# Optimization experiments

Hardware: AMD Instinct MI355X
Metric: run time of the kernel (lower is better)

Reference implementation:

```python
import jax, jax.numpy as jnp
import numpy as np

# Dimensions inferred from VSSBlockOneWay(hidden_dim=256, ssm_d_state=64, forward_type='m0_noz')
B_, L_, D_ = 8, 2048, 256      # batch, seq_len, d_model
DIN, N_, P_ = 512, 64, 64      # d_inner = 2*d_model, d_state, head_dim
H_ = DIN // P_                 # n_heads = 8


def _ln(x, w, b, eps=1e-5):
    m = x.mean(-1, keepdims=True)
    v = ((x - m) ** 2).mean(-1, keepdims=True)
    return (x - m) * jax.lax.rsqrt(v + eps) * w + b


def setup_inputs() -> dict:
    key = jax.random.key(0)
    ks = jax.random.split(key, 8)
    s = lambda k, shape, sc: jax.random.normal(k, shape, jnp.float32) * sc
    return dict(
        src=jax.random.normal(ks[0], (B_, L_, D_), jnp.float32),
        ln_w=jnp.ones((D_,), jnp.float32), ln_b=jnp.zeros((D_,), jnp.float32),
        W_in=s(ks[1], (D_, DIN), 0.02),
        conv_w=s(ks[2], (DIN, 1, 3), 0.1),            # depthwise conv1d kernel
        conv_b=jnp.zeros((DIN,), jnp.float32),
        W_xproj=s(ks[3], (DIN, H_ + 2 * N_), 0.02),   # -> (dt | B | C)
        dt_bias=s(ks[4], (H_,), 0.1),
        A_log=jnp.log(jnp.arange(1, H_ + 1, dtype=jnp.float32)),  # Mamba2 A-init
        Ds=jnp.ones((H_,), jnp.float32),
        oln_w=jnp.ones((DIN,), jnp.float32), oln_b=jnp.zeros((DIN,), jnp.float32),
        W_out=s(ks[5], (DIN, D_), 0.02),
    )


def reference(src, ln_w, ln_b, W_in, conv_w, conv_b, W_xproj, dt_bias,
              A_log, Ds, oln_w, oln_b, W_out):
    B, L, D = src.shape
    H, N, P = H_, N_, P_
    x = _ln(src, ln_w, ln_b)
    u = x @ W_in                                                    # (B,L,DIN)
    # depthwise conv over sequence, SAME padding (VMamba uses non-causal dwconv)
    uc = jax.lax.conv_general_dilated(
        u.transpose(0, 2, 1), conv_w, (1,), 'SAME',
        feature_group_count=DIN, dimension_numbers=('NCH', 'OIH', 'NCH'))
    u = jax.nn.gelu((uc + conv_b[None, :, None]).transpose(0, 2, 1),
                    approximate=False)                              # (B,L,DIN)
    dbc = u @ W_xproj                                               # (B,L,H+2N)
    dt = jax.nn.softplus(dbc[..., :H] + dt_bias)                    # (B,L,H)
    Bm = dbc[..., H:H + N]                                          # (B,L,N)
    Cm = dbc[..., H + N:]                                           # (B,L,N)
    A = -jnp.exp(A_log)                                             # (H,)
    decay = jnp.exp(dt * A)                                         # (B,L,H)
    xh = u.reshape(B, L, H, P)
    dtx = dt[..., None] * xh                                        # (B,L,H,P)

    def step(h, inp):
        dec_t, dtx_t, B_t, C_t = inp
        # h: (B,H,P,N)
        h = h * dec_t[:, :, None, None] + dtx_t[..., None] * B_t[:, None, None, :]
        y = jnp.einsum('bhpn,bn->bhp', h, C_t)
        return h, y

    h0 = jnp.zeros((B, H, P, N), u.dtype)
    inputs = (decay.transpose(1, 0, 2), dtx.transpose(1, 0, 2, 3),
              Bm.transpose(1, 0, 2), Cm.transpose(1, 0, 2))
    _, ys = jax.lax.scan(step, h0, inputs)                          # (L,B,H,P)
    y = ys.transpose(1, 0, 2, 3) + xh * Ds[None, None, :, None]
    y = _ln(y.reshape(B, L, DIN), oln_w, oln_b)
    # dropout / drop_path are identity at inference
    return src + y @ W_out
```

## Files before the change

kernel.cpp:

```cpp
#include <hip/hip_runtime.h>
#include <hip/hip_bf16.h>
#include <cmath>

typedef __hip_bfloat16 bf16;
typedef short bf16x8 __attribute__((ext_vector_type(8)));
typedef short bf16x4v __attribute__((ext_vector_type(4)));
typedef float f32x4 __attribute__((ext_vector_type(4)));

constexpr int B_ = 8, L_ = 2048, D_ = 256, DIN_ = 512;
constexpr int H_ = 8, N_ = 64, P_ = 64;
constexpr int BL_ = B_ * L_;
constexpr int NCH_ = 136;
constexpr int Q_ = 64;
constexpr int NC_ = L_ / Q_;

static __device__ __forceinline__ float b2f(bf16 x) { return __bfloat162float(x); }
static __device__ __forceinline__ bf16  f2b(float x) { return __float2bfloat16(x); }
static __device__ __forceinline__ bf16  rawb(short s) { __hip_bfloat16_raw r; r.x = (unsigned short)s; return (bf16)r; }
static __device__ __forceinline__ float sane(float v) { return (fabsf(v) <= 1e30f) ? v : 0.f; }
static __device__ __forceinline__ float loadx(const void* p, size_t i, bool isbf) {
    return isbf ? b2f(((const bf16*)p)[i]) : ((const float*)p)[i];
}
static __device__ __forceinline__ bf16x8 load8x(const void* p, size_t off, bool isbf) {
    if (isbf) return *(const bf16x8*)((const bf16*)p + off);
    const float4* fp = (const float4*)((const float*)p + off);
    float4 f0 = fp[0], f1 = fp[1];
    bf16 t[8] = {f2b(f0.x), f2b(f0.y), f2b(f0.z), f2b(f0.w),
                 f2b(f1.x), f2b(f1.y), f2b(f1.z), f2b(f1.w)};
    return *(bf16x8*)t;
}
static __device__ __forceinline__ int swz(int row, int col) { return col ^ (((row >> 3) & 7) * 8); }

static __device__ __forceinline__ f32x4 mfma16(bf16x8 a, bf16x8 b, f32x4 c) {
    return __builtin_amdgcn_mfma_f32_16x16x32_bf16(a, b, c, 0, 0, 0);
}
#define ONES8 bf16x8{16256, 16256, 16256, 16256, 16256, 16256, 16256, 16256}

__global__ __launch_bounds__(256) void prep_k(const void* __restrict__ Win, const void* __restrict__ Wx,
                       const void* __restrict__ Wo,
                       const void* __restrict__ ln_w, const void* __restrict__ ln_b,
                       const void* __restrict__ oln_w, const void* __restrict__ oln_b,
                       bf16* __restrict__ WinT, bf16* __restrict__ WxT, bf16* __restrict__ WoT,
                       float* __restrict__ colsum1, float* __restrict__ bias1,
                       float* __restrict__ colsum2, float* __restrict__ bias2,
                       const unsigned short* __restrict__ flagp) {
    const bool isbf = flagp[0] != 0;
    const int bx = blockIdx.x, tid = threadIdx.x;
    if (bx < 88) {
        __shared__ float T[64][65];
        if (bx < 32) {
            int d0 = (bx & 3) * 64, n0 = (bx >> 2) * 64;
#pragma unroll
            for (int i = 0; i < 16; i++) {
                int e = tid + 256 * i; int r = e >> 6, c = e & 63;
                T[r][c] = loadx(Win, (size_t)(d0 + r) * DIN_ + n0 + c, isbf);
            }
            __syncthreads();
#pragma unroll
            for (int i = 0; i < 16; i++) {
                int e = tid + 256 * i; int r = e >> 6, c = e & 63;
                WinT[(size_t)(n0 + r) * D_ + d0 + c] = f2b(loadx(ln_w, d0 + c, isbf) * T[c][r]);
            }
        } else if (bx < 64) {
            int t2 = bx - 32;
            int k0 = (t2 & 7) * 64, d0 = (t2 >> 3) * 64;
#pragma unroll
            for (int i = 0; i < 16; i++) {
                int e = tid + 256 * i; int r = e >> 6, c = e & 63;
                T[r][c] = loadx(Wo, (size_t)(k0 + r) * D_ + d0 + c, isbf);
            }
            __syncthreads();
#pragma unroll
            for (int i = 0; i < 16; i++) {
                int e = tid + 256 * i; int r = e >> 6, c = e & 63;
                WoT[(size_t)(d0 + r) * DIN_ + k0 + c] = f2b(loadx(oln_w, k0 + c, isbf) * T[c][r]);
            }
        } else {
            int t3 = bx - 64;
            int i0 = (t3 & 7) * 64, j0 = (t3 >> 3) * 64;
#pragma unroll
            for (int i = 0; i < 16; i++) {
                int e = tid + 256 * i; int r = e >> 6, c = e & 63;
                int j = j0 + c;
                T[r][c] = (j < NCH_) ? loadx(Wx, (size_t)(i0 + r) * NCH_ + j, isbf) : 0.f;
            }
            __syncthreads();
#pragma unroll
            for (int i = 0; i < 16; i++) {
                int e = tid + 256 * i; int r = e >> 6, c = e & 63;
                WxT[(size_t)(j0 + r) * DIN_ + i0 + c] = f2b(T[c][r]);
            }
        }
        return;
    }
    const int o = (bx - 88) * 4 + (tid >> 6);
    const int lane = tid & 63;
    float cs = 0.f, bs = 0.f;
    if (o < DIN_) {
        int n = o;
        for (int i = lane; i < D_; i += 64) {
            float wv = loadx(Win, (size_t)i * DIN_ + n, isbf);
            cs += loadx(ln_w, i, isbf) * wv;
            bs += loadx(ln_b, i, isbf) * wv;
        }
    } else {
        int d = o - DIN_;
        for (int k = lane; k < DIN_; k += 64) {
            float wv = loadx(Wo, (size_t)k * D_ + d, isbf);
            cs += loadx(oln_w, k, isbf) * wv;
            bs += loadx(oln_b, k, isbf) * wv;
        }
    }
#pragma unroll
    for (int off = 32; off >= 1; off >>= 1) { cs += __shfl_xor(cs, off); bs += __shfl_xor(bs, off); }
    if (lane == 0) {
        if (o < DIN_) { colsum1[o] = cs; bias1[o] = bs; }
        else          { colsum2[o - DIN_] = cs; bias2[o - DIN_] = bs; }
    }
}

__global__ __launch_bounds__(256) void gemm1_k(const void* __restrict__ src,
                                               const bf16* __restrict__ WinT,
                                               const float* __restrict__ colsum1,
                                               const float* __restrict__ bias1,
                                               bf16* __restrict__ u0,
                                               const unsigned short* __restrict__ flagp) {
    const bool isbf = flagp[0] != 0;
    constexpr int K = D_;
    constexpr int STR = K + 8;
    constexpr int CH = K / 8;
    __shared__ bf16 Blds[64 * STR];
    const int tid = threadIdx.x;
    const int n0 = blockIdx.y * 64;
#pragma unroll
    for (int i = 0; i < 64 * CH / 256; i++) {
        int e = tid + 256 * i;
        int r = e / CH, cch = e % CH;
        bf16x8 v = *(const bf16x8*)(WinT + (size_t)(n0 + r) * K + cch * 8);
        *(bf16x8*)(&Blds[r * STR + cch * 8]) = v;
    }
    __syncthreads();
    const int wave = tid >> 6, lane = tid & 63;
    const int quad = lane >> 4, l16 = lane & 15;
    const int m0 = blockIdx.x * 128 + wave * 32;
    const bf16x8 ones = ONES8;
    f32x4 acc[2][4], accS[2], accS2[2];
#pragma unroll
    for (int i = 0; i < 2; i++) {
        accS[i] = f32x4{0.f, 0.f, 0.f, 0.f};
        accS2[i] = f32x4{0.f, 0.f, 0.f, 0.f};
#pragma unroll
        for (int j = 0; j < 4; j++) acc[i][j] = f32x4{0.f, 0.f, 0.f, 0.f};
    }
    const size_t r0 = (size_t)(m0 + l16) * K + quad * 8;
    const size_t r1 = r0 + (size_t)16 * K;
#pragma unroll
    for (int k0 = 0; k0 < K; k0 += 32) {
        bf16x8 a0 = load8x(src, r0 + k0, isbf);
        bf16x8 a1 = load8x(src, r1 + k0, isbf);
        accS[0]  = mfma16(a0, ones, accS[0]);
        accS2[0] = mfma16(a0, a0, accS2[0]);
        accS[1]  = mfma16(a1, ones, accS[1]);
        accS2[1] = mfma16(a1, a1, accS2[1]);
#pragma unroll
        for (int i = 0; i < 4; i++) {
            bf16x8 bb = *(const bf16x8*)(&Blds[(16 * i + l16) * STR + k0 + quad * 8]);
            acc[0][i] = mfma16(a0, bb, acc[0][i]);
            acc[1][i] = mfma16(a1, bb, acc[1][i]);
        }
    }
    float cs[4], bsv[4];
#pragma unroll
    for (int i = 0; i < 4; i++) { int n = n0 + 16 * i + l16; cs[i] = colsum1[n]; bsv[i] = bias1[n]; }
#pragma unroll
    for (int rb = 0; rb < 2; rb++)
#pragma unroll
        for (int r = 0; r < 4; r++) {
            int rl = quad * 4 + r;
            float sv  = accS[rb][r];
            float s2v = __shfl(accS2[rb][r], (quad << 4) + rl);
            float mean = sv * (1.f / D_);
            float var  = s2v * (1.f / D_) - mean * mean;
            float rs = rsqrtf(fmaxf(var, 0.f) + 1e-5f);
            int m = m0 + rb * 16 + rl;
#pragma unroll
            for (int i = 0; i < 4; i++) {
                int n = n0 + 16 * i + l16;
                float v = rs * (acc[rb][i][r] - mean * cs[i]) + bsv[i];
                u0[(size_t)m * DIN_ + n] = f2b(v);
            }
        }
}

template<int MODE>
__global__ __launch_bounds__(256) void gemmB_k(const bf16* __restrict__ A,
                                               const bf16* __restrict__ BT,
                                               void* __restrict__ Cout,
                                               const void* __restrict__ resid,
                                               const float* __restrict__ colsum,
                                               const float* __restrict__ biasv,
                                               const void* __restrict__ dt_bias,
                                               const void* __restrict__ A_log,
                                               float* __restrict__ dtg,
                                               float* __restrict__ dtAg,
                                               const unsigned short* __restrict__ flagp) {
    const bool isbf = flagp[0] != 0;
    constexpr int K = 512;
    constexpr int KH = 256;
    constexpr int STR = KH + 8;
    constexpr int CH = KH / 8;
    __shared__ bf16 Blds[64 * STR];
    const int tid = threadIdx.x;
    const int n0 = blockIdx.y * 64;
    const int wave = tid >> 6, lane = tid & 63;
    const int quad = lane >> 4, l16 = lane & 15;
    const int m0 = blockIdx.x * 128 + wave * 32;
    const bf16x8 ones = ONES8;
    f32x4 acc[2][4], accS[2], accS2[2];
#pragma unroll
    for (int i = 0; i < 2; i++) {
        accS[i] = f32x4{0.f, 0.f, 0.f, 0.f};
        accS2[i] = f32x4{0.f, 0.f, 0.f, 0.f};
#pragma unroll
        for (int j = 0; j < 4; j++) acc[i][j] = f32x4{0.f, 0.f, 0.f, 0.f};
    }
    const bf16* a0p = A + (size_t)(m0 + l16) * K + quad * 8;
    const bf16* a1p = a0p + (size_t)16 * K;
#pragma unroll
    for (int kh = 0; kh < 2; kh++) {
        if (kh) __syncthreads();
#pragma unroll
        for (int i = 0; i < 64 * CH / 256; i++) {
            int e = tid + 256 * i;
            int r = e / CH, cch = e % CH;
            bf16x8 v = *(const bf16x8*)(BT + (size_t)(n0 + r) * K + kh * KH + cch * 8);
            *(bf16x8*)(&Blds[r * STR + cch * 8]) = v;
        }
        __syncthreads();
        const bf16* ah0 = a0p + kh * KH;
        const bf16* ah1 = a1p + kh * KH;
#pragma unroll 4
        for (int k0 = 0; k0 < KH; k0 += 32) {
            bf16x8 a0 = *(const bf16x8*)(ah0 + k0);
            bf16x8 a1 = *(const bf16x8*)(ah1 + k0);
            if (MODE == 1) {
                accS[0]  = mfma16(a0, ones, accS[0]);
                accS2[0] = mfma16(a0, a0, accS2[0]);
                accS[1]  = mfma16(a1, ones, accS[1]);
                accS2[1] = mfma16(a1, a1, accS2[1]);
            }
#pragma unroll
            for (int i = 0; i < 4; i++) {
                bf16x8 bb = *(const bf16x8*)(&Blds[(16 * i + l16) * STR + k0 + quad * 8]);
                acc[0][i] = mfma16(a0, bb, acc[0][i]);
                acc[1][i] = mfma16(a1, bb, acc[1][i]);
            }
        }
    }
    if (MODE == 0) {
#pragma unroll
        for (int rb = 0; rb < 2; rb++)
#pragma unroll
            for (int r = 0; r < 4; r++) {
                int m = m0 + rb * 16 + quad * 4 + r;
#pragma unroll
                for (int i = 0; i < 4; i++) {
                    int n = n0 + 16 * i + l16;
                    if (n < NCH_) ((bf16*)Cout)[(size_t)m * NCH_ + n] = f2b(acc[rb][i][r]);
                }
            }
        if (blockIdx.y == 0 && l16 < 8) {
            float bb = loadx(dt_bias, l16, isbf);
            float Ah = -__expf(fminf(loadx(A_log, l16, isbf), 30.f));
#pragma unroll
            for (int rb = 0; rb < 2; rb++)
#pragma unroll
                for (int r = 0; r < 4; r++) {
                    int m = m0 + rb * 16 + quad * 4 + r;
                    float raw = acc[rb][0][r] + bb;
                    float sp = raw > 20.f ? raw : log1pf(__expf(raw));
                    sp = fminf(sp, 60.f);
                    dtg[(size_t)m * H_ + l16]  = sp;
                    dtAg[(size_t)m * H_ + l16] = sp * Ah;
                }
        }
    } else {
        float cs[4], bsv[4];
#pragma unroll
        for (int i = 0; i < 4; i++) { int n = n0 + 16 * i + l16; cs[i] = colsum[n]; bsv[i] = biasv[n]; }
#pragma unroll
        for (int rb = 0; rb < 2; rb++)
#pragma unroll
            for (int r = 0; r < 4; r++) {
                int rl = quad * 4 + r;
                float sv  = accS[rb][r];
                float s2v = __shfl(accS2[rb][r], (quad << 4) + rl);
                float mean = sv * (1.f / K);
                float var  = s2v * (1.f / K) - mean * mean;
                float rs = rsqrtf(fmaxf(var, 0.f) + 1e-5f);
                int m = m0 + rb * 16 + rl;
#pragma unroll
                for (int i = 0; i < 4; i++) {
                    int n = n0 + 16 * i + l16;
                    size_t o = (size_t)m * D_ + n;
                    float v = rs * (acc[rb][i][r] - mean * cs[i]) + bsv[i] + loadx(resid, o, isbf);
                    v = sane(v);
                    if (isbf) ((bf16*)Cout)[o] = f2b(v);
                    else      ((float*)Cout)[o] = v;
                }
            }
    }
}

constexpr int CSTRIP_ = 4;
__global__ __launch_bounds__(256) void conv_k(const bf16* __restrict__ u0,
                                              const void* __restrict__ cw,
                                              const void* __restrict__ cb,
                                              bf16* __restrict__ u,
                                              const unsigned short* __restrict__ flagp) {
    const bool isbf = flagp[0] != 0;
    __shared__ float wlds[2048];
    {
        int t = threadIdx.x;
#pragma unroll
        for (int i = 0; i < 6; i++) { int e = t + 256 * i; wlds[e] = loadx(cw, e, isbf); }
        wlds[t + 1536] = loadx(cb, t, isbf);
        wlds[t + 1792] = loadx(cb, t + 256, isbf);
    }
    __syncthreads();
    const int wave = threadIdx.x >> 6, lane = threadIdx.x & 63;
    const int sid = blockIdx.x * 4 + wave;
    const int bl0 = sid * CSTRIP_;
    const int l0 = bl0 & (L_ - 1);
    const int c8 = lane * 8;
    float w0[8], w1[8], w2[8], bias[8];
#pragma unroll
    for (int t = 0; t < 8; t++) {
        int ch = c8 + t;
        w0[t] = wlds[ch * 3 + 0];
        w1[t] = wlds[ch * 3 + 1];
        w2[t] = wlds[ch * 3 + 2];
        bias[t] = wlds[1536 + ch];
    }
    const bf16x8* rp = (const bf16x8*)(u0 + (size_t)bl0 * DIN_ + c8);
    bf16x8 zero = {0, 0, 0, 0, 0, 0, 0, 0};
    bf16x8 vl = (l0 > 0) ? rp[-64] : zero;
    bf16x8 vm = rp[0];
#pragma unroll
    for (int i = 0; i < CSTRIP_; i++) {
        int l = l0 + i;
        bf16x8 vr = (l < L_ - 1) ? rp[64 * (i + 1)] : zero;
        bf16 ob[8];
#pragma unroll
        for (int t = 0; t < 8; t++) {
            float a = bias[t] + w1[t] * b2f(rawb(vm[t]))
                    + w0[t] * b2f(rawb(vl[t])) + w2[t] * b2f(rawb(vr[t]));
            float ge = 0.5f * a * (1.f + erff(a * 0.70710678118f));
            ob[t] = f2b(ge);
        }
        *(bf16x8*)(u + (size_t)(bl0 + i) * DIN_ + c8) = *(bf16x8*)ob;
        vl = vm; vm = vr;
    }
}

__global__ __launch_bounds__(256) void chunk_state_k(const bf16* __restrict__ ubuf,
                                                     const bf16* __restrict__ dbcb,
                                                     const float* __restrict__ dtg,
                                                     const float* __restrict__ dtAg,
                                                     bf16* __restrict__ HS,
                                                     float* __restrict__ cdg) {
    const int idx = blockIdx.x;
    const int c = idx & 31, h = (idx >> 5) & 7, b = idx >> 8;
    const int bh = b * 8 + h;
    const int blbase = b * L_ + c * Q_;
    __shared__ bf16 Xw[64][72];
    __shared__ bf16 BTb[64][72];
    __shared__ float fj[64];
    const int tid = threadIdx.x;
    if (tid < 64) {
        int j = tid;
        float dA  = dtAg[(size_t)(blbase + j) * H_ + h];
        float dtv = dtg[(size_t)(blbase + j) * H_ + h];
        float v = dA;
#pragma unroll
        for (int off = 1; off < 64; off <<= 1) { float t = __shfl_up(v, off); if (j >= off) v += t; }
        float segEnd = __shfl(v, 63);
        fj[j] = __expf(fminf(segEnd - v, 0.f)) * dtv;
        if (j == 0) cdg[bh * NC_ + c] = __expf(fminf(segEnd, 0.f));
    }
    __syncthreads();
    {
        const int jr = tid >> 3, p8 = (tid & 7) * 8;
#pragma unroll
        for (int it = 0; it < 2; it++) {
            int j = jr + 32 * it;
            float fs = fj[j];
            bf16x8 xv = *(const bf16x8*)(ubuf + (size_t)(blbase + j) * DIN_ + h * 64 + p8);
            bf16x8 bv = *(const bf16x8*)(dbcb + (size_t)(blbase + j) * NCH_ + 8 + p8);
#pragma unroll
            for (int t = 0; t < 8; t++) {
                int p = p8 + t;
                Xw[p][swz(p, j)]  = f2b(fs * b2f(rawb(xv[t])));
                BTb[p][swz(p, j)] = rawb(bv[t]);
            }
        }
    }
    __syncthreads();
    const int wave = tid >> 6, lane = tid & 63, quad = lane >> 4, l16 = lane & 15;
    const int p0 = wave * 16;
    f32x4 acc[4];
#pragma unroll
    for (int i = 0; i < 4; i++) acc[i] = f32x4{0.f, 0.f, 0.f, 0.f};
#pragma unroll
    for (int ks = 0; ks < 2; ks++) {
        int pa = p0 + l16;
        bf16x8 a = *(const bf16x8*)(&Xw[pa][swz(pa, ks * 32 + quad * 8)]);
#pragma unroll
        for (int nt = 0; nt < 4; nt++) {
            int nb = nt * 16 + l16;
            bf16x8 bb = *(const bf16x8*)(&BTb[nb][swz(nb, ks * 32 + quad * 8)]);
            acc[nt] = mfma16(a, bb, acc[nt]);
        }
    }
    size_t slot = (size_t)(bh * NC_ + c) * 4096;
#pragma unroll
    for (int nt = 0; nt < 4; nt++)
#pragma unroll
        for (int r = 0; r < 4; r++) {
            int p = p0 + quad * 4 + r, n = nt * 16 + l16;
            HS[slot + p * 64 + n] = f2b(sane(acc[nt][r]));
        }
}

__global__ __launch_bounds__(256) void chunk_rec_k(bf16* __restrict__ HS,
                                                   const float* __restrict__ cdg) {
    const int bh = blockIdx.x >> 2, sub = blockIdx.x & 3;
    const int eo = sub * 1024 + threadIdx.x * 4;
    bf16* base = HS + (size_t)bh * (NC_ * 4096) + eo;
    bf16x4v v[NC_];
#pragma unroll
    for (int c = 0; c < NC_; c++) v[c] = *(const bf16x4v*)(base + (size_t)c * 4096);
    float cdr[NC_];
#pragma unroll
    for (int c = 0; c < NC_; c++) cdr[c] = cdg[bh * NC_ + c];
    float h0 = 0.f, h1 = 0.f, h2 = 0.f, h3 = 0.f;
#pragma unroll
    for (int c = 0; c < NC_; c++) {
        bf16 ob[4] = {f2b(h0), f2b(h1), f2b(h2), f2b(h3)};
        *(bf16x4v*)(base + (size_t)c * 4096) = *(bf16x4v*)ob;
        float cd = cdr[c];
        h0 = cd * h0 + b2f(rawb(v[c][0]));
        h1 = cd * h1 + b2f(rawb(v[c][1]));
        h2 = cd * h2 + b2f(rawb(v[c][2]));
        h3 = cd * h3 + b2f(rawb(v[c][3]));
    }
}

__global__ __launch_bounds__(256) void chunk_out_k(bf16* __restrict__ ubuf,
                                                   const bf16* __restrict__ dbcb,
                                                   const float* __restrict__ dtg,
                                                   const float* __restrict__ dtAg,
                                                   const bf16* __restrict__ HS,
                                                   const void* __restrict__ Ds,
                                                   bf16* __restrict__ ybuf,
                                                   const unsigned short* __restrict__ flagp) {
    const bool isbf = flagp[0] != 0;
    const int idx = blockIdx.x;
    const int c = idx & 31, h = (idx >> 5) & 7, b = idx >> 8;
    const int bh = b * 8 + h;
    const int blbase = b * L_ + c * Q_;
    const size_t slotbase = (size_t)(bh * NC_ + c) * 4096;
    __shared__ bf16 Xb[64][72];
    __shared__ bf16 Gb[64][72];
    __shared__ float segL[64], PL[64], dtL[64];
    const int tid = threadIdx.x;
    if (tid < 64) {
        int j = tid;
        float dA  = dtAg[(size_t)(blbase + j) * H_ + h];
        float dtv = dtg[(size_t)(blbase + j) * H_ + h];
        float v = dA;
#pragma unroll
        for (int off = 1; off < 64; off <<= 1) { float t = __shfl_up(v, off); if (j >= off) v += t; }
        segL[j] = v;
        PL[j]   = __expf(fminf(v, 0.f));
        dtL[j]  = dtv;
    }
    {
        const int rr = tid >> 3, k8 = (tid & 7) * 8;
#pragma unroll
        for (int it = 0; it < 2; it++) {
            int r = rr + 32 * it;
            bf16x8 xv = *(const bf16x8*)(ubuf + (size_t)(blbase + r) * DIN_ + h * 64 + k8);
#pragma unroll
            for (int t = 0; t < 8; t++) { int p = k8 + t; Xb[p][swz(p, r)] = rawb(xv[t]); }
        }
    }
    __syncthreads();
    const int wave = tid >> 6, lane = tid & 63, quad = lane >> 4, l16 = lane & 15;
    const int l0 = wave * 16;
    f32x4 g[4];
#pragma unroll
    for (int i = 0; i < 4; i++) g[i] = f32x4{0.f, 0.f, 0.f, 0.f};
#pragma unroll
    for (int ks = 0; ks < 2; ks++) {
        bf16x8 a = *(const bf16x8*)(dbcb + (size_t)(blbase + l0 + l16) * NCH_ + 72 + ks * 32 + quad * 8);
#pragma unroll
        for (int jt = 0; jt < 4; jt++) {
            bf16x8 bb = *(const bf16x8*)(dbcb + (size_t)(blbase + jt * 16 + l16) * NCH_ + 8 + ks * 32 + quad * 8);
            g[jt] = mfma16(a, bb, g[jt]);
        }
    }
#pragma unroll
    for (int jt = 0; jt < 4; jt++) {
        int j = jt * 16 + l16;
#pragma unroll
        for (int r = 0; r < 4; r++) {
            int l = l0 + quad * 4 + r;
            float e = __expf(fminf(segL[l] - segL[j], 0.f));
            float gv = (j <= l) ? sane(g[jt][r]) * e * dtL[j] : 0.f;
            Gb[l][swz(l, j)] = f2b(sane(gv));
        }
    }
    __syncthreads();
    f32x4 y1[4], y2[4];
#pragma unroll
    for (int i = 0; i < 4; i++) { y1[i] = f32x4{0.f, 0.f, 0.f, 0.f}; y2[i] = f32x4{0.f, 0.f, 0.f, 0.f}; }
#pragma unroll
    for (int ks = 0; ks < 2; ks++) {
        int la = l0 + l16;
        bf16x8 ag = *(const bf16x8*)(&Gb[la][swz(la, ks * 32 + quad * 8)]);
        bf16x8 ac = *(const bf16x8*)(dbcb + (size_t)(blbase + la) * NCH_ + 72 + ks * 32 + quad * 8);
#pragma unroll
        for (int pt = 0; pt < 4; pt++) {
            int pb = pt * 16 + l16;
            bf16x8 bx = *(const bf16x8*)(&Xb[pb][swz(pb, ks * 32 + quad * 8)]);
            bf16x8 bhf = *(const bf16x8*)(HS + slotbase + (size_t)pb * 64 + ks * 32 + quad * 8);
            y1[pt] = mfma16(ag, bx, y1[pt]);
            y2[pt] = mfma16(ac, bhf, y2[pt]);
        }
    }
    float dsH = loadx(Ds, h, isbf);
#pragma unroll
    for (int pt = 0; pt < 4; pt++) {
        int p = pt * 16 + l16;
#pragma unroll
        for (int r = 0; r < 4; r++) {
            int l = l0 + quad * 4 + r;
            float yv = y1[pt][r] + PL[l] * y2[pt][r] + dsH * b2f(Xb[p][swz(p, l)]);
            ybuf[(size_t)(blbase + l) * DIN_ + h * 64 + p] = f2b(sane(yv));
        }
    }
}

extern "C" void kernel_launch(void* const* d_in, const int* in_sizes, int n_in,
                              void* d_out, int out_size, void* d_ws, size_t ws_size,
                              hipStream_t stream) {
    const void* src     = d_in[0];
    const void* ln_w    = d_in[1];
    const void* ln_b    = d_in[2];
    const void* W_in    = d_in[3];
    const void* conv_w  = d_in[4];
    const void* conv_b  = d_in[5];
    const void* W_xproj = d_in[6];
    const void* dt_bias = d_in[7];
    const void* A_log   = d_in[8];
    const void* Ds      = d_in[9];
    const void* oln_w   = d_in[10];
    const void* oln_b   = d_in[11];
    const void* W_out   = d_in[12];
    const unsigned short* flagp = (const unsigned short*)ln_w;

    char* w = (char*)d_ws;
    size_t off = 0;
    auto alloc = [&](size_t bytes) { void* p = w + off; off += (bytes + 255) & ~(size_t)255; return p; };
    char*   regB   = (char*)alloc((size_t)BL_ * DIN_ * 2);
    char*   regC   = (char*)alloc((size_t)BL_ * DIN_ * 2);
    bf16*   dbcb   = (bf16*)alloc((size_t)BL_ * NCH_ * 2);
    float*  dtg    = (float*)alloc((size_t)BL_ * H_ * 4);
    float*  dtAg   = (float*)alloc((size_t)BL_ * H_ * 4);
    bf16*   WinT   = (bf16*)alloc((size_t)DIN_ * D_ * 2);
    bf16*   WxT    = (bf16*)alloc((size_t)192 * DIN_ * 2);
    bf16*   WoT    = (bf16*)alloc((size_t)D_ * DIN_ * 2);
    float*  colsum1= (float*)alloc(DIN_ * 4);
    float*  bias1  = (float*)alloc(DIN_ * 4);
    float*  colsum2= (float*)alloc(D_ * 4);
    float*  bias2  = (float*)alloc(D_ * 4);
    float*  cdg    = (float*)alloc((size_t)64 * NC_ * 4);

    bf16* u0buf = (bf16*)regB;
    bf16* HS    = (bf16*)regB;
    bf16* ubuf  = (bf16*)regC;
    bf16* ybuf  = (bf16*)regC;

    prep_k<<<88 + 192, 256, 0, stream>>>(W_in, W_xproj, W_out, ln_w, ln_b, oln_w, oln_b,
                                         WinT, WxT, WoT, colsum1, bias1, colsum2, bias2, flagp);
    gemm1_k<<<dim3(BL_ / 128, 8), 256, 0, stream>>>(src, WinT, colsum1, bias1, u0buf, flagp);
    conv_k<<<BL_ / CSTRIP_ / 4, 256, 0, stream>>>(u0buf, conv_w, conv_b, ubuf, flagp);
    gemmB_k<0><<<dim3(BL_ / 128, 3), 256, 0, stream>>>(ubuf, WxT, dbcb, nullptr, nullptr, nullptr,
                                                       dt_bias, A_log, dtg, dtAg, flagp);
    chunk_state_k<<<B_ * H_ * NC_, 256, 0, stream>>>(ubuf, dbcb, dtg, dtAg, HS, cdg);
    chunk_rec_k<<<256, 256, 0, stream>>>(HS, cdg);
    chunk_out_k<<<B_ * H_ * NC_, 256, 0, stream>>>(ubuf, dbcb, dtg, dtAg, HS, Ds, ybuf, flagp);
    gemmB_k<1><<<dim3(BL_ / 128, 4), 256, 0, stream>>>(ybuf, WoT, d_out, src, colsum2, bias2,
                                                       nullptr, nullptr, nullptr, nullptr, flagp);
}
```

Baseline: 199.0 us.

## Fuse input GEMM with depthwise conv and GELU via LDS halo rows

Merges the LayerNorm+input-projection GEMM with the depthwise conv and GELU into one kernel. The GEMM tile is staged in shared memory, and the two halo rows at the tile edges are recomputed with a scalar dot product over the staged weight slice. This removes the intermediate u0 write and read plus one kernel launch. In exchange it adds extra shared memory per block, serial halo work for 128 threads, and another barrier.

```diff
diff --git a/kernel.cpp b/kernel.cpp
--- a/kernel.cpp
+++ b/kernel.cpp
@@ -119,19 +119,24 @@
     }
 }
 
-__global__ __launch_bounds__(256) void gemm1_k(const void* __restrict__ src,
-                                               const bf16* __restrict__ WinT,
-                                               const float* __restrict__ colsum1,
-                                               const float* __restrict__ bias1,
-                                               bf16* __restrict__ u0,
-                                               const unsigned short* __restrict__ flagp) {
+__global__ __launch_bounds__(256) void gemm1conv_k(const void* __restrict__ src,
+                                                   const bf16* __restrict__ WinT,
+                                                   const float* __restrict__ colsum1,
+                                                   const float* __restrict__ bias1,
+                                                   const void* __restrict__ cw,
+                                                   const void* __restrict__ cb,
+                                                   bf16* __restrict__ u,
+                                                   const unsigned short* __restrict__ flagp) {
     const bool isbf = flagp[0] != 0;
     constexpr int K = D_;
     constexpr int STR = K + 8;
     constexpr int CH = K / 8;
     __shared__ bf16 Blds[64 * STR];
+    __shared__ bf16 U[130][72];
     const int tid = threadIdx.x;
     const int n0 = blockIdx.y * 64;
+    const int m0 = blockIdx.x * 128;
+    const int l0i = m0 & (L_ - 1);
 #pragma unroll
     for (int i = 0; i < 64 * CH / 256; i++) {
         int e = tid + 256 * i;
@@ -142,7 +147,7 @@
     __syncthreads();
     const int wave = tid >> 6, lane = tid & 63;
     const int quad = lane >> 4, l16 = lane & 15;
-    const int m0 = blockIdx.x * 128 + wave * 32;
+    const int mw = m0 + wave * 32;
     const bf16x8 ones = ONES8;
     f32x4 acc[2][4], accS[2], accS2[2];
 #pragma unroll
@@ -152,7 +157,7 @@
 #pragma unroll
         for (int j = 0; j < 4; j++) acc[i][j] = f32x4{0.f, 0.f, 0.f, 0.f};
     }
-    const size_t r0 = (size_t)(m0 + l16) * K + quad * 8;
+    const size_t r0 = (size_t)(mw + l16) * K + quad * 8;
     const size_t r1 = r0 + (size_t)16 * K;
 #pragma unroll
     for (int k0 = 0; k0 < K; k0 += 32) {
@@ -182,14 +187,67 @@
             float mean = sv * (1.f / D_);
             float var  = s2v * (1.f / D_) - mean * mean;
             float rs = rsqrtf(fmaxf(var, 0.f) + 1e-5f);
-            int m = m0 + rb * 16 + rl;
+            int rloc = wave * 32 + rb * 16 + rl;
 #pragma unroll
             for (int i = 0; i < 4; i++) {
-                int n = n0 + 16 * i + l16;
                 float v = rs * (acc[rb][i][r] - mean * cs[i]) + bsv[i];
-                u0[(size_t)m * DIN_ + n] = f2b(v);
-            }
-        }
+                U[1 + rloc][16 * i + l16] = f2b(v);
+            }
+        }
+    if (tid < 128) {
+        const int hrow = tid >> 6;
+        const int n = tid & 63;
+        const int urow = hrow ? 129 : 0;
+        const bool valid = hrow ? (l0i != L_ - 128) : (l0i != 0);
+        float val = 0.f;
+        if (valid) {
+            const int g = hrow ? (m0 + 128) : (m0 - 1);
+            const bf16* brow = &Blds[n * STR];
+            float dot = 0.f, s = 0.f, s2 = 0.f;
+            for (int k8 = 0; k8 < CH; k8++) {
+                bf16x8 bb = *(const bf16x8*)(brow + k8 * 8);
+#pragma unroll
+                for (int t = 0; t < 8; t++) {
+                    float a = b2f(f2b(loadx(src, (size_t)g * K + k8 * 8 + t, isbf)));
+                    dot += a * b2f(rawb(bb[t]));
+                    s += a; s2 += a * a;
+                }
+            }
+            float mean = s * (1.f / D_);
+            float var  = s2 * (1.f / D_) - mean * mean;
+            float rs = rsqrtf(fmaxf(var, 0.f) + 1e-5f);
+            val = rs * (dot - mean * colsum1[n0 + n]) + bias1[n0 + n];
+        }
+        U[urow][n] = f2b(val);
+    }
+    __syncthreads();
+    const int cg = tid & 7, rg = tid >> 3;
+    const int c8 = cg * 8;
+    float w0[8], w1[8], w2[8], bia[8];
+#pragma unroll
+    for (int t = 0; t < 8; t++) {
+        int chn = n0 + c8 + t;
+        w0[t]  = loadx(cw, chn * 3 + 0, isbf);
+        w1[t]  = loadx(cw, chn * 3 + 1, isbf);
+        w2[t]  = loadx(cw, chn * 3 + 2, isbf);
+        bia[t] = loadx(cb, chn, isbf);
+    }
+#pragma unroll
+    for (int i = 0; i < 4; i++) {
+        int r = rg * 4 + i;
+        bf16x8 vl = *(const bf16x8*)(&U[r][c8]);
+        bf16x8 vm = *(const bf16x8*)(&U[r + 1][c8]);
+        bf16x8 vr = *(const bf16x8*)(&U[r + 2][c8]);
+        bf16 ob[8];
+#pragma unroll
+        for (int t = 0; t < 8; t++) {
+            float a = bia[t] + w1[t] * b2f(rawb(vm[t]))
+                    + w0[t] * b2f(rawb(vl[t])) + w2[t] * b2f(rawb(vr[t]));
+            float ge = 0.5f * a * (1.f + erff(a * 0.70710678118f));
+            ob[t] = f2b(ge);
+        }
+        *(bf16x8*)(u + (size_t)(m0 + r) * DIN_ + n0 + c8) = *(bf16x8*)ob;
+    }
 }
 
 template<int MODE>
@@ -312,57 +370,6 @@
     }
 }
 
-constexpr int CSTRIP_ = 4;
-__global__ __launch_bounds__(256) void conv_k(const bf16* __restrict__ u0,
-                                              const void* __restrict__ cw,
-                                              const void* __restrict__ cb,
-                                              bf16* __restrict__ u,
-                                              const unsigned short* __restrict__ flagp) {
-    const bool isbf = flagp[0] != 0;
-    __shared__ float wlds[2048];
-    {
-        int t = threadIdx.x;
-#pragma unroll
-        for (int i = 0; i < 6; i++) { int e = t + 256 * i; wlds[e] = loadx(cw, e, isbf); }
-        wlds[t + 1536] = loadx(cb, t, isbf);
-        wlds[t + 1792] = loadx(cb, t + 256, isbf);
-    }
-    __syncthreads();
-    const int wave = threadIdx.x >> 6, lane = threadIdx.x & 63;
-    const int sid = blockIdx.x * 4 + wave;
-    const int bl0 = sid * CSTRIP_;
-    const int l0 = bl0 & (L_ - 1);
-    const int c8 = lane * 8;
-    float w0[8], w1[8], w2[8], bias[8];
-#pragma unroll
-    for (int t = 0; t < 8; t++) {
-        int ch = c8 + t;
-        w0[t] = wlds[ch * 3 + 0];
-        w1[t] = wlds[ch * 3 + 1];
-        w2[t] = wlds[ch * 3 + 2];
-        bias[t] = wlds[1536 + ch];
-    }
-    const bf16x8* rp = (const bf16x8*)(u0 + (size_t)bl0 * DIN_ + c8);
-    bf16x8 zero = {0, 0, 0, 0, 0, 0, 0, 0};
-    bf16x8 vl = (l0 > 0) ? rp[-64] : zero;
-    bf16x8 vm = rp[0];
-#pragma unroll
-    for (int i = 0; i < CSTRIP_; i++) {
-        int l = l0 + i;
-        bf16x8 vr = (l < L_ - 1) ? rp[64 * (i + 1)] : zero;
-        bf16 ob[8];
-#pragma unroll
-        for (int t = 0; t < 8; t++) {
-            float a = bias[t] + w1[t] * b2f(rawb(vm[t]))
-                    + w0[t] * b2f(rawb(vl[t])) + w2[t] * b2f(rawb(vr[t]));
-            float ge = 0.5f * a * (1.f + erff(a * 0.70710678118f));
-            ob[t] = f2b(ge);
-        }
-        *(bf16x8*)(u + (size_t)(bl0 + i) * DIN_ + c8) = *(bf16x8*)ob;
-        vl = vm; vm = vr;
-    }
-}
-
 __global__ __launch_bounds__(256) void chunk_state_k(const bf16* __restrict__ ubuf,
                                                      const bf16* __restrict__ dbcb,
                                                      const float* __restrict__ dtg,
@@ -587,15 +594,14 @@
     float*  bias2  = (float*)alloc(D_ * 4);
     float*  cdg    = (float*)alloc((size_t)64 * NC_ * 4);
 
-    bf16* u0buf = (bf16*)regB;
     bf16* HS    = (bf16*)regB;
     bf16* ubuf  = (bf16*)regC;
     bf16* ybuf  = (bf16*)regC;
 
     prep_k<<<88 + 192, 256, 0, stream>>>(W_in, W_xproj, W_out, ln_w, ln_b, oln_w, oln_b,
                                          WinT, WxT, WoT, colsum1, bias1, colsum2, bias2, flagp);
-    gemm1_k<<<dim3(BL_ / 128, 8), 256, 0, stream>>>(src, WinT, colsum1, bias1, u0buf, flagp);
-    conv_k<<<BL_ / CSTRIP_ / 4, 256, 0, stream>>>(u0buf, conv_w, conv_b, ubuf, flagp);
+    gemm1conv_k<<<dim3(BL_ / 128, 8), 256, 0, stream>>>(src, WinT, colsum1, bias1,
+                                                        conv_w, conv_b, ubuf, flagp);
     gemmB_k<0><<<dim3(BL_ / 128, 3), 256, 0, stream>>>(ubuf, WxT, dbcb, nullptr, nullptr, nullptr,
                                                        dt_bias, A_log, dtg, dtAg, flagp);
     chunk_state_k<<<B_ * H_ * NC_, 256, 0, stream>>>(ubuf, dbcb, dtg, dtAg, HS, cdg);
```

Measured after the change: 242.1 us. 1.22x slower.
